# Kernel optimization log

Measured on AMD Instinct MI355X. Metric: run time of the kernel, lower is better.

Reference implementation:

```python
import jax, jax.numpy as jnp
import numpy as np

B, N, DIM, H = 32, 3136, 768, 12
C = DIM // H  # head_dim = 64


def setup_inputs() -> dict:
    key = jax.random.key(0)
    k1, k2, k3, k4 = jax.random.split(key, 4)
    x = jax.random.normal(k1, (B, N, DIM), dtype=jnp.float32)
    # Linear weights stored as (in, out); qkv has no bias (qkv_bias=False)
    w_qkv = jax.random.normal(k2, (DIM, 3 * DIM), dtype=jnp.float32) * (1.0 / np.sqrt(DIM))
    w_proj = jax.random.normal(k3, (DIM, DIM), dtype=jnp.float32) * (1.0 / np.sqrt(DIM))
    b_proj = jax.random.normal(k4, (DIM,), dtype=jnp.float32) * 0.01
    return {"x": x, "w_qkv": w_qkv, "w_proj": w_proj, "b_proj": b_proj}


def reference(x, w_qkv, w_proj, b_proj):
    # qkv projection: [B,N,3*DIM] -> [3,B,H,N,C]
    qkv = (x @ w_qkv).reshape(B, N, 3, H, C).transpose(2, 0, 3, 1, 4)
    q, k, v = qkv[0], qkv[1], qkv[2]
    # Efficient (linear) attention: softmax q over channel dim, k over token dim
    q = jax.nn.softmax(q, axis=-1)                      # [B,H,N,C], softmax over C
    kt = jax.nn.softmax(k.transpose(0, 1, 3, 2), axis=-1)  # [B,H,C,N], softmax over N
    context = jnp.einsum('bhcn,bhnd->bhcd', kt, v)      # [B,H,C,C]
    out = jnp.einsum('bhnc,bhcd->bhnd', q, context)     # [B,H,N,C]
    out = out.transpose(0, 2, 1, 3).reshape(B, N, DIM)  # [B,N,DIM]
    return out @ w_proj + b_proj
```

## Files before the change

kernel.cpp:

```cpp
#include <hip/hip_runtime.h>
#include <hip/hip_bf16.h>

typedef __attribute__((ext_vector_type(8))) short bf16x8;
typedef __attribute__((ext_vector_type(4))) float f32x4;

constexpr int BATCH = 32, SEQ = 3136, DIM = 768, NH = 12, HD = 64;
constexpr int M_TOT = BATCH * SEQ;
constexpr int QKVC  = 3 * DIM;
constexpr int GK    = 768;

__device__ __forceinline__ float bf2f(unsigned short u) {
  union { unsigned int i; float f; } x; x.i = ((unsigned int)u) << 16; return x.f;
}
__device__ __forceinline__ unsigned short f2bf(float f) {
  union { float f; unsigned int i; } x; x.f = f;
  unsigned int r = x.i + 0x7FFFu + ((x.i >> 16) & 1u);
  return (unsigned short)(r >> 16);
}
__device__ __forceinline__ unsigned int pack2(float lo, float hi) {
  return (unsigned int)f2bf(lo) | ((unsigned int)f2bf(hi) << 16);
}
__device__ __forceinline__ void gload_lds16(const unsigned short* g, unsigned short* l) {
  __builtin_amdgcn_global_load_lds(
      (const __attribute__((address_space(1))) void*)g,
      (__attribute__((address_space(3))) void*)l, 16, 0, 0);
}

#define BARX()  asm volatile("s_barrier" ::: "memory")
#define LGKM0() asm volatile("s_waitcnt lgkmcnt(0)" ::: "memory")
#define VM8()   asm volatile("s_waitcnt vmcnt(8)" ::: "memory")
#define VM6()   asm volatile("s_waitcnt vmcnt(6)" ::: "memory")
#define SB0()   __builtin_amdgcn_sched_barrier(0)

__global__ void conv_kernel(const float* __restrict__ in, unsigned short* __restrict__ out, long n) {
  long i = ((long)blockIdx.x * blockDim.x + threadIdx.x) * 8;
  long stride = (long)gridDim.x * blockDim.x * 8;
  for (; i < n; i += stride) {
    float4 a = *(const float4*)(in + i);
    float4 b = *(const float4*)(in + i + 4);
    uint4 o;
    o.x = pack2(a.x, a.y); o.y = pack2(a.z, a.w);
    o.z = pack2(b.x, b.y); o.w = pack2(b.z, b.w);
    *(uint4*)(out + i) = o;
  }
}

__global__ void transp_kernel(const float* __restrict__ w, unsigned short* __restrict__ wt, int K, int N) {
  __shared__ float tile[32][33];
  int n0 = blockIdx.x * 32, k0 = blockIdx.y * 32;
  int tx = threadIdx.x, ty = threadIdx.y;
  #pragma unroll
  for (int i = 0; i < 32; i += 8)
    tile[ty + i][tx] = w[(size_t)(k0 + ty + i) * N + n0 + tx];
  __syncthreads();
  #pragma unroll
  for (int i = 0; i < 32; i += 8)
    wt[(size_t)(n0 + ty + i) * K + k0 + tx] = f2bf(tile[tx][ty + i]);
}

__device__ __forceinline__ void stage_half(const unsigned short* __restrict__ G, long row0, int col0,
                                           unsigned short* ldsHalf, int t) {
  int r = t >> 2;
  int gslot = (t & 3) ^ ((t >> 3) & 3);
  char* dst = (char*)ldsHalf + ((t >> 6) << 10);
  gload_lds16(G + (row0 + r) * (long)GK + col0 + gslot * 8, (unsigned short*)dst);
  gload_lds16(G + (row0 + 128 + r) * (long)GK + col0 + gslot * 8, (unsigned short*)(dst + 8192));
}
__device__ __forceinline__ bf16x8 frag(const unsigned short* half, int r, int ko) {
  return *(const bf16x8*)((const char*)half + r * 64 + ((((ko >> 3) ^ ((r >> 1) & 3))) << 4));
}

#define MM16G(Q,A0,A1,A2,A3,B0,B1,B2,B3) do { \
  acc[(Q)+0][0]=__builtin_amdgcn_mfma_f32_16x16x32_bf16(A0,B0,acc[(Q)+0][0],0,0,0); \
  acc[(Q)+0][1]=__builtin_amdgcn_mfma_f32_16x16x32_bf16(A0,B1,acc[(Q)+0][1],0,0,0); \
  acc[(Q)+0][2]=__builtin_amdgcn_mfma_f32_16x16x32_bf16(A0,B2,acc[(Q)+0][2],0,0,0); \
  acc[(Q)+0][3]=__builtin_amdgcn_mfma_f32_16x16x32_bf16(A0,B3,acc[(Q)+0][3],0,0,0); \
  acc[(Q)+1][0]=__builtin_amdgcn_mfma_f32_16x16x32_bf16(A1,B0,acc[(Q)+1][0],0,0,0); \
  acc[(Q)+1][1]=__builtin_amdgcn_mfma_f32_16x16x32_bf16(A1,B1,acc[(Q)+1][1],0,0,0); \
  acc[(Q)+1][2]=__builtin_amdgcn_mfma_f32_16x16x32_bf16(A1,B2,acc[(Q)+1][2],0,0,0); \
  acc[(Q)+1][3]=__builtin_amdgcn_mfma_f32_16x16x32_bf16(A1,B3,acc[(Q)+1][3],0,0,0); \
  acc[(Q)+2][0]=__builtin_amdgcn_mfma_f32_16x16x32_bf16(A2,B0,acc[(Q)+2][0],0,0,0); \
  acc[(Q)+2][1]=__builtin_amdgcn_mfma_f32_16x16x32_bf16(A2,B1,acc[(Q)+2][1],0,0,0); \
  acc[(Q)+2][2]=__builtin_amdgcn_mfma_f32_16x16x32_bf16(A2,B2,acc[(Q)+2][2],0,0,0); \
  acc[(Q)+2][3]=__builtin_amdgcn_mfma_f32_16x16x32_bf16(A2,B3,acc[(Q)+2][3],0,0,0); \
  acc[(Q)+3][0]=__builtin_amdgcn_mfma_f32_16x16x32_bf16(A3,B0,acc[(Q)+3][0],0,0,0); \
  acc[(Q)+3][1]=__builtin_amdgcn_mfma_f32_16x16x32_bf16(A3,B1,acc[(Q)+3][1],0,0,0); \
  acc[(Q)+3][2]=__builtin_amdgcn_mfma_f32_16x16x32_bf16(A3,B2,acc[(Q)+3][2],0,0,0); \
  acc[(Q)+3][3]=__builtin_amdgcn_mfma_f32_16x16x32_bf16(A3,B3,acc[(Q)+3][3],0,0,0); \
} while (0)

#define KTILE_W(BUF, MA2, NB2, C2, MA3, NB3, C3) { \
  const unsigned short* Ah0 = &lds[BUF][0][0][0]; \
  const unsigned short* Bh1 = &lds[BUF][1][1][0]; \
  const unsigned short* Ah1 = &lds[BUF][0][1][0]; \
  const unsigned short* Ah0n = &lds[(BUF) ^ 1][0][0][0]; \
  const unsigned short* Bh0n = &lds[(BUF) ^ 1][1][0][0]; \
   \
  LGKM0(); SB0(); \
  __builtin_amdgcn_s_setprio(1); MM16G(0, a0, a1, a2, a3, b0, b1, b2, b3); \
  __builtin_amdgcn_s_setprio(0); SB0(); \
  a4 = frag(Ah0, ra + 64, ko); a5 = frag(Ah0, ra + 80, ko); \
  a6 = frag(Ah0, ra + 96, ko); a7 = frag(Ah0, ra + 112, ko); \
  stage_half(A, MA2, C2, &lds[(BUF) ^ 1][0][1][0], t); \
  VM6(); BARX(); \
   \
  LGKM0(); SB0(); \
  __builtin_amdgcn_s_setprio(1); MM16G(4, a4, a5, a6, a7, b0, b1, b2, b3); \
  __builtin_amdgcn_s_setprio(0); SB0(); \
  a0 = frag(Ah1, ra,      ko); a1 = frag(Ah1, ra + 16, ko); \
  a2 = frag(Ah1, ra + 32, ko); a3 = frag(Ah1, ra + 48, ko); \
  b4 = frag(Bh1, rb,      ko); b5 = frag(Bh1, rb + 16, ko); \
  b6 = frag(Bh1, rb + 32, ko); b7 = frag(Bh1, rb + 48, ko); \
  stage_half(Bt, NB2, C2, &lds[(BUF) ^ 1][1][1][0], t); \
  BARX(); \
   \
  LGKM0(); SB0(); \
  __builtin_amdgcn_s_setprio(1); MM16G(0, a0, a1, a2, a3, b4, b5, b6, b7); \
  __builtin_amdgcn_s_setprio(0); SB0(); \
  a4 = frag(Ah1, ra + 64, ko); a5 = frag(Ah1, ra + 80, ko); \
  a6 = frag(Ah1, ra + 96, ko); a7 = frag(Ah1, ra + 112, ko); \
  stage_half(A, MA3, C3, &lds[BUF][0][0][0], t); \
  VM6(); BARX(); \
   \
  LGKM0(); SB0(); \
  __builtin_amdgcn_s_setprio(1); MM16G(4, a4, a5, a6, a7, b4, b5, b6, b7); \
  __builtin_amdgcn_s_setprio(0); SB0(); \
  a0 = frag(Ah0n, ra,      ko); a1 = frag(Ah0n, ra + 16, ko); \
  a2 = frag(Ah0n, ra + 32, ko); a3 = frag(Ah0n, ra + 48, ko); \
  b0 = frag(Bh0n, rb,      ko); b1 = frag(Bh0n, rb + 16, ko); \
  b2 = frag(Bh0n, rb + 32, ko); b3 = frag(Bh0n, rb + 48, ko); \
  stage_half(Bt, NB3, C3, &lds[BUF][1][0][0], t); \
  BARX(); \
}

template<int OUTMODE, int NT>
__global__ __launch_bounds__(512, 2) void gemm256p(const unsigned short* __restrict__ A,
                                                   const unsigned short* __restrict__ Bt,
                                                   void* __restrict__ Cp,
                                                   const float* __restrict__ bias,
                                                   int Nld, int TPX) {
  __shared__ unsigned short lds[2][2][2][8192];
  int t = threadIdx.x, lane = t & 63, wid = t >> 6;
  int wm = wid >> 2, wn = wid & 3;
  int bid = (int)blockIdx.x;
  int xcd = bid & 7, slot = bid >> 3;
  int tau = xcd * TPX + slot;
  int tend = (xcd + 1) * TPX;
  int fl = lane & 15, ko = (lane >> 4) * 8;
  int ra = wm * 128 + fl, rb = wn * 64 + fl;
  f32x4 acc[8][4];
  bf16x8 a0, a1, a2, a3, a4, a5, a6, a7, b0, b1, b2, b3, b4, b5, b6, b7;
  {
    long m0 = (long)(tau / NT) * 256, n0 = (long)(tau % NT) * 256;
    stage_half(A,  m0, 0,  &lds[0][0][0][0], t);
    stage_half(Bt, n0, 0,  &lds[0][1][0][0], t);
    stage_half(A,  m0, 32, &lds[0][0][1][0], t);
    stage_half(Bt, n0, 32, &lds[0][1][1][0], t);
    stage_half(A,  m0, 64, &lds[1][0][0][0], t);
    stage_half(Bt, n0, 64, &lds[1][1][0][0], t);
    VM8(); BARX();
    a0 = frag(&lds[0][0][0][0], ra,      ko); a1 = frag(&lds[0][0][0][0], ra + 16, ko);
    a2 = frag(&lds[0][0][0][0], ra + 32, ko); a3 = frag(&lds[0][0][0][0], ra + 48, ko);
    b0 = frag(&lds[0][1][0][0], rb,      ko); b1 = frag(&lds[0][1][0][0], rb + 16, ko);
    b2 = frag(&lds[0][1][0][0], rb + 32, ko); b3 = frag(&lds[0][1][0][0], rb + 48, ko);
  }
  #pragma unroll 1
  for (; tau < tend; tau += 32) {
    long m0 = (long)(tau / NT) * 256, n0 = (long)(tau % NT) * 256;
    int tn = (tau + 32 < tend) ? tau + 32 : tau;
    long m0n = (long)(tn / NT) * 256, n0n = (long)(tn % NT) * 256;
    #pragma unroll
    for (int i = 0; i < 8; ++i)
      #pragma unroll
      for (int j2 = 0; j2 < 4; ++j2) acc[i][j2] = (f32x4){0.f, 0.f, 0.f, 0.f};
    #pragma unroll 1
    for (int j = 0; j < 10; j += 2) {
      KTILE_W(0, m0, n0, j * 64 + 96,  m0, n0, j * 64 + 128);
      KTILE_W(1, m0, n0, j * 64 + 160, m0, n0, j * 64 + 192);
    }
    KTILE_W(0, m0,  n0,  736, m0n, n0n, 0);
    KTILE_W(1, m0n, n0n, 32,  m0n, n0n, 64);
    int r0 = (lane >> 4) * 4;
    #pragma unroll
    for (int mf = 0; mf < 8; ++mf) {
      #pragma unroll
      for (int nf = 0; nf < 4; ++nf) {
        long row = m0 + wm * 128 + mf * 16 + r0;
        int col = (int)n0 + wn * 64 + nf * 16 + fl;
        if (OUTMODE == 0) {
          unsigned short* C = (unsigned short*)Cp;
          bool doexp = (n0 < 2 * DIM);
          #pragma unroll
          for (int r = 0; r < 4; ++r) {
            float v = acc[mf][nf][r];
            C[(size_t)(row + r) * Nld + col] = f2bf(doexp ? __expf(v) : v);
          }
        } else {
          float* C = (float*)Cp;
          float bb = bias[col];
          #pragma unroll
          for (int r = 0; r < 4; ++r)
            C[(size_t)(row + r) * Nld + col] = acc[mf][nf][r] + bb;
        }
      }
    }
  }
}

__global__ void ctx_part(const unsigned short* __restrict__ qkv, float* __restrict__ part,
                         float* __restrict__ dpart) {
  int blk = blockIdx.x;
  int bh = blk / 7, ch = blk - bh * 7;
  int b = bh / NH, h = bh % NH;
  __shared__ unsigned short Et[64 * 40];
  __shared__ unsigned short Vt[64 * 40];
  __shared__ float denom[64];
  int t = threadIdx.x, lane = t & 63, w = t >> 6;
  if (t < 64) denom[t] = 0.0f;
  int nl = t >> 3, e0 = (t & 7) * 8;
  int ko = (lane >> 4) * 8, fl = lane & 15;
  size_t base = (size_t)b * SEQ * QKVC + (size_t)h * HD;
  float dp[8] = {};
  f32x4 acc[4] = {};
  int c0b = ch * 448;
  for (int c0 = c0b; c0 < c0b + 448; c0 += 32) {
    __syncthreads();
    size_t rb = base + (size_t)(c0 + nl) * QKVC;
    uint4 kvec = *(const uint4*)(qkv + rb + DIM + e0);
    uint4 vvec = *(const uint4*)(qkv + rb + 2 * DIM + e0);
    const unsigned short* kp = (const unsigned short*)&kvec;
    const unsigned short* vp = (const unsigned short*)&vvec;
    #pragma unroll
    for (int j = 0; j < 8; ++j) {
      dp[j] += bf2f(kp[j]);
      Et[(e0 + j) * 40 + nl] = kp[j];
      Vt[(e0 + j) * 40 + nl] = vp[j];
    }
    __syncthreads();
    bf16x8 af = *(const bf16x8*)(Et + (w * 16 + fl) * 40 + ko);
    #pragma unroll
    for (int nf = 0; nf < 4; ++nf) {
      bf16x8 bv = *(const bf16x8*)(Vt + (nf * 16 + fl) * 40 + ko);
      acc[nf] = __builtin_amdgcn_mfma_f32_16x16x32_bf16(af, bv, acc[nf], 0, 0, 0);
    }
  }
  #pragma unroll
  for (int j = 0; j < 8; ++j) atomicAdd(&denom[e0 + j], dp[j]);
  __syncthreads();
  int r0 = (lane >> 4) * 4;
  float* pp = part + (size_t)blk * 4096;
  #pragma unroll
  for (int nf = 0; nf < 4; ++nf)
    #pragma unroll
    for (int r = 0; r < 4; ++r) {
      int c = w * 16 + r0 + r;
      int d = nf * 16 + fl;
      pp[d * 64 + c] = acc[nf][r];
    }
  if (t < 64) dpart[blk * 64 + t] = denom[t];
}

__global__ void ctx_reduce(const float* __restrict__ part, const float* __restrict__ dpart,
                           unsigned short* __restrict__ ctxT) {
  int bh = blockIdx.x, t = threadIdx.x;
  const float* pp = part + (size_t)bh * 7 * 4096;
  const float* dd = dpart + (size_t)bh * 7 * 64;
  #pragma unroll
  for (int i = 0; i < 16; ++i) {
    int idx = i * 256 + t;
    float s = 0.f, ds = 0.f;
    #pragma unroll
    for (int c = 0; c < 7; ++c) {
      s += pp[c * 4096 + idx];
      ds += dd[c * 64 + (idx & 63)];
    }
    ctxT[(size_t)bh * 4096 + idx] = f2bf(s / ds);
  }
}

__global__ void pv_kernel(const unsigned short* __restrict__ qkv, const unsigned short* __restrict__ ctxT,
                          unsigned short* __restrict__ aout) {
  int bid = blockIdx.x;
  int bh = bid / 49, chunk = bid - bh * 49;
  int b = bh / NH, h = bh % NH;
  int n0 = chunk * 64;
  __shared__ unsigned short P[64 * 80];
  __shared__ unsigned short CT[64 * 80];
  __shared__ float srow[64];
  int t = threadIdx.x, lane = t & 63, w = t >> 6;
  int ko = (lane >> 4) * 8, fl = lane & 15;
  if (t < 64) srow[t] = 0.0f;
  {
    int d = t >> 2, cq = (t & 3) * 16;
    const uint4* src = (const uint4*)(ctxT + (size_t)bh * 4096 + d * 64 + cq);
    *(uint4*)(CT + d * 80 + cq) = src[0];
    *(uint4*)(CT + d * 80 + cq + 8) = src[1];
  }
  __syncthreads();
  {
    int nl = t >> 2, cq = (t & 3) * 16;
    size_t rb = (size_t)(b * SEQ + n0 + nl) * QKVC + h * HD + cq;
    uint4 q0 = *(const uint4*)(qkv + rb);
    uint4 q1 = *(const uint4*)(qkv + rb + 8);
    *(uint4*)(P + nl * 80 + cq) = q0;
    *(uint4*)(P + nl * 80 + cq + 8) = q1;
    const unsigned short* qp0 = (const unsigned short*)&q0;
    const unsigned short* qp1 = (const unsigned short*)&q1;
    float s = 0.0f;
    #pragma unroll
    for (int j = 0; j < 8; ++j) s += bf2f(qp0[j]) + bf2f(qp1[j]);
    atomicAdd(&srow[nl], s);
  }
  __syncthreads();
  f32x4 acc[4] = {};
  #pragma unroll
  for (int kk = 0; kk < 2; ++kk) {
    bf16x8 af = *(const bf16x8*)(P + (w * 16 + fl) * 80 + kk * 32 + ko);
    #pragma unroll
    for (int nf = 0; nf < 4; ++nf) {
      bf16x8 bv = *(const bf16x8*)(CT + (nf * 16 + fl) * 80 + kk * 32 + ko);
      acc[nf] = __builtin_amdgcn_mfma_f32_16x16x32_bf16(af, bv, acc[nf], 0, 0, 0);
    }
  }
  int r0 = (lane >> 4) * 4;
  #pragma unroll
  for (int nf = 0; nf < 4; ++nf)
    #pragma unroll
    for (int r = 0; r < 4; ++r) {
      int nlr = w * 16 + r0 + r;
      int d = nf * 16 + fl;
      float v = acc[nf][r] / srow[nlr];
      aout[(size_t)(b * SEQ + n0 + nlr) * DIM + h * HD + d] = f2bf(v);
    }
}

extern "C" void kernel_launch(void* const* d_in, const int* in_sizes, int n_in,
                              void* d_out, int out_size, void* d_ws, size_t ws_size,
                              hipStream_t stream) {
  const float* x      = (const float*)d_in[0];
  const float* w_qkv  = (const float*)d_in[1];
  const float* w_proj = (const float*)d_in[2];
  const float* b_proj = (const float*)d_in[3];
  char* ws = (char*)d_ws;
  unsigned short* x_bf    = (unsigned short*)(ws);
  unsigned short* wt_qkv  = (unsigned short*)(ws + 154140672);
  unsigned short* wt_proj = (unsigned short*)(ws + 157679616);
  unsigned short* qkv     = (unsigned short*)(ws + 158859264);
  unsigned short* ctxT    = (unsigned short*)(ws + 154140672);
  float* part  = (float*)(ws);
  float* dpart = (float*)(ws + 44040192);
  unsigned short* aout = (unsigned short*)(ws);

  conv_kernel<<<2048, 256, 0, stream>>>(x, x_bf, (long)M_TOT * DIM);
  transp_kernel<<<dim3(QKVC / 32, DIM / 32), dim3(32, 8), 0, stream>>>(w_qkv, wt_qkv, DIM, QKVC);
  transp_kernel<<<dim3(DIM / 32, DIM / 32), dim3(32, 8), 0, stream>>>(w_proj, wt_proj, DIM, DIM);
  gemm256p<0, 9><<<256, 512, 0, stream>>>(x_bf, wt_qkv, qkv, nullptr, QKVC, 441);
  ctx_part<<<BATCH * NH * 7, 256, 0, stream>>>(qkv, part, dpart);
  ctx_reduce<<<BATCH * NH, 256, 0, stream>>>(part, dpart, ctxT);
  pv_kernel<<<BATCH * NH * (SEQ / 64), 256, 0, stream>>>(qkv, ctxT, aout);
  gemm256p<1, 3><<<256, 512, 0, stream>>>(aout, wt_proj, (float*)d_out, b_proj, DIM, 147);
}
```

Baseline: 801.4 us.

## Swap MFMA operands for row-contiguous epilogue stores and retune pipeline waits

Swaps the A/B operands of every MFMA so each lane's accumulator holds four consecutive output columns of one row. The epilogue can then write packed 8-byte bf16 or 16-byte float stores, and read bias as a float4, instead of four scattered scalar stores. The per-stage B fragment loads and the vmcnt waits are also reshuffled (vmcnt 4 after B staging instead of vmcnt 6 after A staging) to change how the LDS prefetch overlaps. The risk is a correctness hazard if the new wait placement lets fragments be read before their global-to-LDS loads land.

New measurement: 860.6 us. 1.07x slower.

```diff
diff --git a/kernel.cpp b/kernel.cpp
--- a/kernel.cpp
+++ b/kernel.cpp
@@ -28,8 +28,7 @@
 
 #define BARX()  asm volatile("s_barrier" ::: "memory")
 #define LGKM0() asm volatile("s_waitcnt lgkmcnt(0)" ::: "memory")
-#define VM8()   asm volatile("s_waitcnt vmcnt(8)" ::: "memory")
-#define VM6()   asm volatile("s_waitcnt vmcnt(6)" ::: "memory")
+#define VM4()   asm volatile("s_waitcnt vmcnt(4)" ::: "memory")
 #define SB0()   __builtin_amdgcn_sched_barrier(0)
 
 __global__ void conv_kernel(const float* __restrict__ in, unsigned short* __restrict__ out, long n) {
@@ -71,28 +70,28 @@
 }
 
 #define MM16G(Q,A0,A1,A2,A3,B0,B1,B2,B3) do { \
-  acc[(Q)+0][0]=__builtin_amdgcn_mfma_f32_16x16x32_bf16(A0,B0,acc[(Q)+0][0],0,0,0); \
-  acc[(Q)+0][1]=__builtin_amdgcn_mfma_f32_16x16x32_bf16(A0,B1,acc[(Q)+0][1],0,0,0); \
-  acc[(Q)+0][2]=__builtin_amdgcn_mfma_f32_16x16x32_bf16(A0,B2,acc[(Q)+0][2],0,0,0); \
-  acc[(Q)+0][3]=__builtin_amdgcn_mfma_f32_16x16x32_bf16(A0,B3,acc[(Q)+0][3],0,0,0); \
-  acc[(Q)+1][0]=__builtin_amdgcn_mfma_f32_16x16x32_bf16(A1,B0,acc[(Q)+1][0],0,0,0); \
-  acc[(Q)+1][1]=__builtin_amdgcn_mfma_f32_16x16x32_bf16(A1,B1,acc[(Q)+1][1],0,0,0); \
-  acc[(Q)+1][2]=__builtin_amdgcn_mfma_f32_16x16x32_bf16(A1,B2,acc[(Q)+1][2],0,0,0); \
-  acc[(Q)+1][3]=__builtin_amdgcn_mfma_f32_16x16x32_bf16(A1,B3,acc[(Q)+1][3],0,0,0); \
-  acc[(Q)+2][0]=__builtin_amdgcn_mfma_f32_16x16x32_bf16(A2,B0,acc[(Q)+2][0],0,0,0); \
-  acc[(Q)+2][1]=__builtin_amdgcn_mfma_f32_16x16x32_bf16(A2,B1,acc[(Q)+2][1],0,0,0); \
-  acc[(Q)+2][2]=__builtin_amdgcn_mfma_f32_16x16x32_bf16(A2,B2,acc[(Q)+2][2],0,0,0); \
-  acc[(Q)+2][3]=__builtin_amdgcn_mfma_f32_16x16x32_bf16(A2,B3,acc[(Q)+2][3],0,0,0); \
-  acc[(Q)+3][0]=__builtin_amdgcn_mfma_f32_16x16x32_bf16(A3,B0,acc[(Q)+3][0],0,0,0); \
-  acc[(Q)+3][1]=__builtin_amdgcn_mfma_f32_16x16x32_bf16(A3,B1,acc[(Q)+3][1],0,0,0); \
-  acc[(Q)+3][2]=__builtin_amdgcn_mfma_f32_16x16x32_bf16(A3,B2,acc[(Q)+3][2],0,0,0); \
-  acc[(Q)+3][3]=__builtin_amdgcn_mfma_f32_16x16x32_bf16(A3,B3,acc[(Q)+3][3],0,0,0); \
+  acc[(Q)+0][0]=__builtin_amdgcn_mfma_f32_16x16x32_bf16(B0,A0,acc[(Q)+0][0],0,0,0); \
+  acc[(Q)+0][1]=__builtin_amdgcn_mfma_f32_16x16x32_bf16(B1,A0,acc[(Q)+0][1],0,0,0); \
+  acc[(Q)+0][2]=__builtin_amdgcn_mfma_f32_16x16x32_bf16(B2,A0,acc[(Q)+0][2],0,0,0); \
+  acc[(Q)+0][3]=__builtin_amdgcn_mfma_f32_16x16x32_bf16(B3,A0,acc[(Q)+0][3],0,0,0); \
+  acc[(Q)+1][0]=__builtin_amdgcn_mfma_f32_16x16x32_bf16(B0,A1,acc[(Q)+1][0],0,0,0); \
+  acc[(Q)+1][1]=__builtin_amdgcn_mfma_f32_16x16x32_bf16(B1,A1,acc[(Q)+1][1],0,0,0); \
+  acc[(Q)+1][2]=__builtin_amdgcn_mfma_f32_16x16x32_bf16(B2,A1,acc[(Q)+1][2],0,0,0); \
+  acc[(Q)+1][3]=__builtin_amdgcn_mfma_f32_16x16x32_bf16(B3,A1,acc[(Q)+1][3],0,0,0); \
+  acc[(Q)+2][0]=__builtin_amdgcn_mfma_f32_16x16x32_bf16(B0,A2,acc[(Q)+2][0],0,0,0); \
+  acc[(Q)+2][1]=__builtin_amdgcn_mfma_f32_16x16x32_bf16(B1,A2,acc[(Q)+2][1],0,0,0); \
+  acc[(Q)+2][2]=__builtin_amdgcn_mfma_f32_16x16x32_bf16(B2,A2,acc[(Q)+2][2],0,0,0); \
+  acc[(Q)+2][3]=__builtin_amdgcn_mfma_f32_16x16x32_bf16(B3,A2,acc[(Q)+2][3],0,0,0); \
+  acc[(Q)+3][0]=__builtin_amdgcn_mfma_f32_16x16x32_bf16(B0,A3,acc[(Q)+3][0],0,0,0); \
+  acc[(Q)+3][1]=__builtin_amdgcn_mfma_f32_16x16x32_bf16(B1,A3,acc[(Q)+3][1],0,0,0); \
+  acc[(Q)+3][2]=__builtin_amdgcn_mfma_f32_16x16x32_bf16(B2,A3,acc[(Q)+3][2],0,0,0); \
+  acc[(Q)+3][3]=__builtin_amdgcn_mfma_f32_16x16x32_bf16(B3,A3,acc[(Q)+3][3],0,0,0); \
 } while (0)
 
-#define KTILE_W(BUF, MA2, NB2, C2, MA3, NB3, C3) { \
+#define KTILE_X(BUF, MA2, NB2, C2, MA3, NB3, C3) { \
   const unsigned short* Ah0 = &lds[BUF][0][0][0]; \
+  const unsigned short* Ah1 = &lds[BUF][0][1][0]; \
   const unsigned short* Bh1 = &lds[BUF][1][1][0]; \
-  const unsigned short* Ah1 = &lds[BUF][0][1][0]; \
   const unsigned short* Ah0n = &lds[(BUF) ^ 1][0][0][0]; \
   const unsigned short* Bh0n = &lds[(BUF) ^ 1][1][0][0]; \
    \
@@ -101,36 +100,36 @@
   __builtin_amdgcn_s_setprio(0); SB0(); \
   a4 = frag(Ah0, ra + 64, ko); a5 = frag(Ah0, ra + 80, ko); \
   a6 = frag(Ah0, ra + 96, ko); a7 = frag(Ah0, ra + 112, ko); \
+  b4 = frag(Bh1, rb, ko); b5 = frag(Bh1, rb + 16, ko); \
   stage_half(A, MA2, C2, &lds[(BUF) ^ 1][0][1][0], t); \
-  VM6(); BARX(); \
+  BARX(); \
    \
   LGKM0(); SB0(); \
   __builtin_amdgcn_s_setprio(1); MM16G(4, a4, a5, a6, a7, b0, b1, b2, b3); \
   __builtin_amdgcn_s_setprio(0); SB0(); \
   a0 = frag(Ah1, ra,      ko); a1 = frag(Ah1, ra + 16, ko); \
   a2 = frag(Ah1, ra + 32, ko); a3 = frag(Ah1, ra + 48, ko); \
-  b4 = frag(Bh1, rb,      ko); b5 = frag(Bh1, rb + 16, ko); \
   b6 = frag(Bh1, rb + 32, ko); b7 = frag(Bh1, rb + 48, ko); \
   stage_half(Bt, NB2, C2, &lds[(BUF) ^ 1][1][1][0], t); \
-  BARX(); \
+  VM4(); BARX(); \
    \
   LGKM0(); SB0(); \
   __builtin_amdgcn_s_setprio(1); MM16G(0, a0, a1, a2, a3, b4, b5, b6, b7); \
   __builtin_amdgcn_s_setprio(0); SB0(); \
   a4 = frag(Ah1, ra + 64, ko); a5 = frag(Ah1, ra + 80, ko); \
   a6 = frag(Ah1, ra + 96, ko); a7 = frag(Ah1, ra + 112, ko); \
+  b0 = frag(Bh0n, rb, ko); b1 = frag(Bh0n, rb + 16, ko); \
   stage_half(A, MA3, C3, &lds[BUF][0][0][0], t); \
-  VM6(); BARX(); \
+  BARX(); \
    \
   LGKM0(); SB0(); \
   __builtin_amdgcn_s_setprio(1); MM16G(4, a4, a5, a6, a7, b4, b5, b6, b7); \
   __builtin_amdgcn_s_setprio(0); SB0(); \
   a0 = frag(Ah0n, ra,      ko); a1 = frag(Ah0n, ra + 16, ko); \
   a2 = frag(Ah0n, ra + 32, ko); a3 = frag(Ah0n, ra + 48, ko); \
-  b0 = frag(Bh0n, rb,      ko); b1 = frag(Bh0n, rb + 16, ko); \
   b2 = frag(Bh0n, rb + 32, ko); b3 = frag(Bh0n, rb + 48, ko); \
   stage_half(Bt, NB3, C3, &lds[BUF][1][0][0], t); \
-  BARX(); \
+  VM4(); BARX(); \
 }
 
 template<int OUTMODE, int NT>
@@ -158,7 +157,7 @@
     stage_half(Bt, n0, 32, &lds[0][1][1][0], t);
     stage_half(A,  m0, 64, &lds[1][0][0][0], t);
     stage_half(Bt, n0, 64, &lds[1][1][0][0], t);
-    VM8(); BARX();
+    VM4(); BARX();
     a0 = frag(&lds[0][0][0][0], ra,      ko); a1 = frag(&lds[0][0][0][0], ra + 16, ko);
     a2 = frag(&lds[0][0][0][0], ra + 32, ko); a3 = frag(&lds[0][0][0][0], ra + 48, ko);
     b0 = frag(&lds[0][1][0][0], rb,      ko); b1 = frag(&lds[0][1][0][0], rb + 16, ko);
@@ -175,32 +174,31 @@
       for (int j2 = 0; j2 < 4; ++j2) acc[i][j2] = (f32x4){0.f, 0.f, 0.f, 0.f};
     #pragma unroll 1
     for (int j = 0; j < 10; j += 2) {
-      KTILE_W(0, m0, n0, j * 64 + 96,  m0, n0, j * 64 + 128);
-      KTILE_W(1, m0, n0, j * 64 + 160, m0, n0, j * 64 + 192);
-    }
-    KTILE_W(0, m0,  n0,  736, m0n, n0n, 0);
-    KTILE_W(1, m0n, n0n, 32,  m0n, n0n, 64);
-    int r0 = (lane >> 4) * 4;
+      KTILE_X(0, m0, n0, j * 64 + 96,  m0, n0, j * 64 + 128);
+      KTILE_X(1, m0, n0, j * 64 + 160, m0, n0, j * 64 + 192);
+    }
+    KTILE_X(0, m0,  n0,  736, m0n, n0n, 0);
+    KTILE_X(1, m0n, n0n, 32,  m0n, n0n, 64);
+    int q4 = (lane >> 4) * 4;
     #pragma unroll
     for (int mf = 0; mf < 8; ++mf) {
+      long row = m0 + wm * 128 + mf * 16 + fl;
       #pragma unroll
       for (int nf = 0; nf < 4; ++nf) {
-        long row = m0 + wm * 128 + mf * 16 + r0;
-        int col = (int)n0 + wn * 64 + nf * 16 + fl;
+        int col = (int)n0 + wn * 64 + nf * 16 + q4;
         if (OUTMODE == 0) {
           unsigned short* C = (unsigned short*)Cp;
           bool doexp = (n0 < 2 * DIM);
-          #pragma unroll
-          for (int r = 0; r < 4; ++r) {
-            float v = acc[mf][nf][r];
-            C[(size_t)(row + r) * Nld + col] = f2bf(doexp ? __expf(v) : v);
-          }
+          float v0 = acc[mf][nf][0], v1 = acc[mf][nf][1], v2 = acc[mf][nf][2], v3 = acc[mf][nf][3];
+          if (doexp) { v0 = __expf(v0); v1 = __expf(v1); v2 = __expf(v2); v3 = __expf(v3); }
+          uint2 o; o.x = pack2(v0, v1); o.y = pack2(v2, v3);
+          *(uint2*)(C + (size_t)row * Nld + col) = o;
         } else {
           float* C = (float*)Cp;
-          float bb = bias[col];
-          #pragma unroll
-          for (int r = 0; r < 4; ++r)
-            C[(size_t)(row + r) * Nld + col] = acc[mf][nf][r] + bb;
+          float4 bb = *(const float4*)(bias + col);
+          float4 o = { acc[mf][nf][0] + bb.x, acc[mf][nf][1] + bb.y,
+                       acc[mf][nf][2] + bb.z, acc[mf][nf][3] + bb.w };
+          *(float4*)(C + (size_t)row * Nld + col) = o;
         }
       }
     }
```
